# Optimization experiments

Hardware: AMD Instinct MI355X
Metric: run time of the kernel (lower is better)

The kernel has to match this reference:

```python
import jax, jax.numpy as jnp
import numpy as np

B, T, N, C = 32, 16, 1000, 16   # batch, seq_len, num_nodes, in_channels
G, H, O = 32, 512, 8            # gcn_hidden, lstm_hidden, output_dim
E_RAND = 8000                   # random edges; + N self loops -> E = 9000


def setup_inputs() -> dict:
    key = jax.random.key(0)
    ks = jax.random.split(key, 13)
    rng = np.random.default_rng(0)
    src = rng.integers(0, N, E_RAND)
    dst = rng.integers(0, N, E_RAND)
    loop = np.arange(N)
    edge_index = jnp.asarray(
        np.stack([np.concatenate([src, loop]), np.concatenate([dst, loop])]),
        dtype=jnp.int32)
    ew = np.concatenate([rng.uniform(0.5, 1.5, E_RAND), np.ones(N)]).astype(np.float32)

    def p(k, s, sc):
        return jax.random.normal(k, s, jnp.float32) * sc

    return {
        'x': p(ks[0], (B, T, N, C), 1.0),
        'edge_index': edge_index,
        'edge_weight': jnp.asarray(ew),
        'gcn_w': p(ks[1], (T, C, G), 0.1),
        'gcn_b': p(ks[2], (T, G), 0.02),
        'w_ih0': p(ks[3], (4 * H, N * G), 0.02),
        'w_hh0': p(ks[4], (4 * H, H), 0.02),
        'b_ih0': p(ks[5], (4 * H,), 0.02),
        'b_hh0': p(ks[6], (4 * H,), 0.02),
        'w_ih1': p(ks[7], (4 * H, H), 0.02),
        'w_hh1': p(ks[8], (4 * H, H), 0.02),
        'b_ih1': p(ks[9], (4 * H,), 0.02),
        'b_hh1': p(ks[10], (4 * H,), 0.02),
        'proj_w': p(ks[11], (O, H), 0.04),
        'proj_b': p(ks[12], (O,), 0.02),
    }


def _lstm_layer(inp, w_ih, w_hh, b_ih, b_hh):
    # inp: [B, T, D]; torch gate order i, f, g, o
    pre = jnp.einsum('btd,gd->btg', inp, w_ih) + b_ih + b_hh  # [B, T, 4H]
    h0 = jnp.zeros((inp.shape[0], w_hh.shape[1]), inp.dtype)

    def step(carry, x_t):
        h, c = carry
        gates = x_t + h @ w_hh.T
        i, f, g, o = jnp.split(gates, 4, axis=-1)
        c = jax.nn.sigmoid(f) * c + jax.nn.sigmoid(i) * jnp.tanh(g)
        h = jax.nn.sigmoid(o) * jnp.tanh(c)
        return (h, c), h

    _, hs = jax.lax.scan(step, (h0, h0), pre.transpose(1, 0, 2))  # [T, B, H]
    return hs.transpose(1, 0, 2)


def reference(x, edge_index, edge_weight, gcn_w, gcn_b,
              w_ih0, w_hh0, b_ih0, b_hh0,
              w_ih1, w_hh1, b_ih1, b_hh1, proj_w, proj_b):
    src, dst = edge_index[0], edge_index[1]
    # GCN symmetric normalization (self-loops already present in edge list)
    deg = jax.ops.segment_sum(edge_weight, dst, num_segments=N)
    dinv = jnp.where(deg > 0, jax.lax.rsqrt(jnp.maximum(deg, 1e-12)), 0.0)
    norm = dinv[src] * edge_weight * dinv[dst]  # [E]
    # per-timestep linear transform: distinct GCN weight per t
    xw = jnp.einsum('btni,tio->btno', x, gcn_w)  # [B, T, N, G]
    # gather from source nodes, scale, scatter-add into targets
    msg = xw[:, :, src, :] * norm[None, None, :, None]      # [B, T, E, G]
    agg = jnp.zeros_like(xw).at[:, :, dst, :].add(msg)      # [B, T, N, G]
    h = jax.nn.relu(agg + gcn_b[None, :, None, :])
    seq = h.reshape(B, T, N * G)                            # [B, T, N*G]
    out1 = _lstm_layer(seq, w_ih0, w_hh0, b_ih0, b_hh0)
    out2 = _lstm_layer(out1, w_ih1, w_hh1, b_ih1, b_hh1)
    last = out2[:, -1, :]                                   # [B, H]
    return last @ proj_w.T + proj_b                         # [B, O]
```

## Files before the change

### kernel.cpp

```cpp
#include <hip/hip_runtime.h>
#include <hip/hip_bf16.h>

typedef unsigned short u16;
typedef __bf16 bf16x8 __attribute__((ext_vector_type(8)));
typedef float f32x4 __attribute__((ext_vector_type(4)));
typedef unsigned short u16x8 __attribute__((ext_vector_type(8)));
typedef unsigned long long u64;

#define NB 32
#define NT 16
#define NN 1000
#define NC 16
#define NG 32
#define NH 512
#define NK 32000
#define BH (NB*NH)
#define LWG 64
#define LTH 384

__device__ __forceinline__ u16 f2bf(float f) {
    unsigned int u = __float_as_uint(f);
    unsigned int r = u + 0x7FFFu + ((u >> 16) & 1u);
    return (u16)(r >> 16);
}

__device__ __forceinline__ float sigmoidf(float x) { return 1.f / (1.f + __expf(-x)); }

__device__ __forceinline__ float dot4(float4 a, float4 b) {
    return a.x * b.x + a.y * b.y + a.z * b.z + a.w * b.w;
}

#define AT_LOAD(p)    __hip_atomic_load((p), __ATOMIC_RELAXED, __HIP_MEMORY_SCOPE_AGENT)
#define AT_STORE(p,v) __hip_atomic_store((p), (v), __ATOMIC_RELAXED, __HIP_MEMORY_SCOPE_AGENT)

#define GLOAD16(g, l) __builtin_amdgcn_global_load_lds( \
    (const __attribute__((address_space(1))) void*)(g),  \
    (__attribute__((address_space(3))) void*)(l), 16, 0, 0)

__global__ void graph_prep(const int* __restrict__ ei, const float* __restrict__ ew, int E,
                           int* __restrict__ rowptr, int* __restrict__ csr_src,
                           float* __restrict__ csr_nrm) {
    __shared__ float degs[NN];
    __shared__ float dinv[NN];
    __shared__ int cnt[NN];
    __shared__ int rp[NN + 1];
    int tid = threadIdx.x;
    for (int n = tid; n < NN; n += 1024) { degs[n] = 0.f; cnt[n] = 0; }
    __syncthreads();
    for (int e = tid; e < E; e += 1024) {
        int d = ei[E + e];
        atomicAdd(&degs[d], ew[e]);
        atomicAdd(&cnt[d], 1);
    }
    __syncthreads();
    for (int n = tid; n < NN; n += 1024) {
        float d = degs[n];
        dinv[n] = d > 0.f ? rsqrtf(fmaxf(d, 1e-12f)) : 0.f;
    }
    __syncthreads();
    if (tid == 0) {
        int acc = 0;
        for (int n = 0; n < NN; ++n) { rp[n] = acc; acc += cnt[n]; }
        rp[NN] = acc;
    }
    __syncthreads();
    for (int n = tid; n <= NN; n += 1024) rowptr[n] = rp[n];
    for (int n = tid; n < NN; n += 1024) cnt[n] = 0;
    __syncthreads();
    for (int e = tid; e < E; e += 1024) {
        int d = ei[E + e], s = ei[e];
        int pos = rp[d] + atomicAdd(&cnt[d], 1);
        csr_src[pos] = s;
        csr_nrm[pos] = dinv[s] * ew[e] * dinv[d];
    }
}

__global__ __launch_bounds__(1024) void gcn_fused(const float* __restrict__ x,
                                                  const float* __restrict__ gw,
                                                  const float* __restrict__ gb,
                                                  const int* __restrict__ rowptr,
                                                  const int* __restrict__ csr_src,
                                                  const float* __restrict__ csr_nrm,
                                                  u16* __restrict__ seq) {
    __shared__ float xwlds[NN * NG];
    __shared__ float wlds[NC * NG];
    __shared__ int rplds[NN + 1];
    int bt = blockIdx.x;
    int t = bt & 15;
    int tid = threadIdx.x;
    int g = tid & 31, grp = tid >> 5;

    for (int i = tid; i < NC * NG; i += 1024) wlds[i] = gw[t * NC * NG + i];
    for (int i = tid; i <= NN; i += 1024) rplds[i] = rowptr[i];
    __syncthreads();

    const float* xbt = x + (size_t)bt * NN * NC;
    for (int r = grp; r < NN; r += 32) {
        const float* xr = xbt + r * NC;
        float acc = 0.f;
#pragma unroll
        for (int i = 0; i < NC; ++i) acc += xr[i] * wlds[i * NG + g];
        xwlds[r * NG + g] = acc;
    }
    __syncthreads();

    float bias = gb[t * NG + g];
    u16* seqbt = seq + (size_t)bt * NK;
    for (int n = grp; n < NN; n += 32) {
        int p0 = rplds[n], p1 = rplds[n + 1];
        float acc = 0.f;
        for (int p = p0; p < p1; ++p)
            acc += csr_nrm[p] * xwlds[csr_src[p] * NG + g];
        seqbt[n * NG + g] = f2bf(fmaxf(acc + bias, 0.f));
    }
}

__global__ void wconv(const float4* __restrict__ in, ushort4* __restrict__ out, int n4) {
    for (int i = blockIdx.x * blockDim.x + threadIdx.x; i < n4; i += gridDim.x * blockDim.x) {
        float4 v = in[i];
        ushort4 o;
        o.x = f2bf(v.x); o.y = f2bf(v.y); o.z = f2bf(v.z); o.w = f2bf(v.w);
        out[i] = o;
    }
}

__global__ __launch_bounds__(256) void gemm_bt(const u16* __restrict__ A,
                                               const u16* __restrict__ Bw,
                                               float* __restrict__ part) {
    __shared__ __align__(16) u16 As[128 * 64];
    __shared__ __align__(16) u16 Bs[128 * 64];
    int tid = threadIdx.x;
    int lane = tid & 63, wid = tid >> 6;
    int wr = wid >> 1, wc = wid & 1;
    int tm = blockIdx.x * 128, tn = blockIdx.y * 128;
    int s = blockIdx.z;
    int ks0 = s * 62 + (s < 4 ? s : 4);
    int ksn = (s < 4) ? 63 : 62;

    int srow = tid >> 3;
    int schunk = tid & 7;

    const u16* ga = A + (size_t)(tm + srow) * NK + (size_t)ks0 * 64 + schunk * 8;
    const u16* gb = Bw + (size_t)(tn + srow) * NK + (size_t)ks0 * 64 + schunk * 8;
    u16* la = As + srow * 64 + schunk * 8;
    u16* lb = Bs + srow * 64 + schunk * 8;

    f32x4 acc[4][4];
#pragma unroll
    for (int i = 0; i < 4; ++i)
#pragma unroll
        for (int j = 0; j < 4; ++j) acc[i][j] = (f32x4){0.f, 0.f, 0.f, 0.f};

    int fr = lane & 15, kq = lane >> 4;
    const u16* arow = As + (wr * 64 + fr) * 64 + kq * 8;
    const u16* brow = Bs + (wc * 64 + fr) * 64 + kq * 8;

    for (int ks = 0; ks < ksn; ++ks) {
        __syncthreads();
#pragma unroll
        for (int q = 0; q < 4; ++q) {
            GLOAD16(ga + (size_t)q * 32 * NK, la + q * 32 * 64);
            GLOAD16(gb + (size_t)q * 32 * NK, lb + q * 32 * 64);
        }
        __syncthreads();
#pragma unroll
        for (int kk = 0; kk < 2; ++kk) {
            bf16x8 af[4], bv[4];
#pragma unroll
            for (int fm = 0; fm < 4; ++fm) af[fm] = *(const bf16x8*)(arow + fm * 1024 + kk * 32);
#pragma unroll
            for (int fn = 0; fn < 4; ++fn) bv[fn] = *(const bf16x8*)(brow + fn * 1024 + kk * 32);
#pragma unroll
            for (int fm = 0; fm < 4; ++fm)
#pragma unroll
                for (int fn = 0; fn < 4; ++fn)
                    acc[fm][fn] = __builtin_amdgcn_mfma_f32_16x16x32_bf16(af[fm], bv[fn], acc[fm][fn], 0, 0, 0);
        }
        ga += 64; gb += 64;
    }

    int rq = lane >> 4;
    size_t base = (size_t)s * 512 * 2048;
#pragma unroll
    for (int fm = 0; fm < 4; ++fm)
#pragma unroll
        for (int fn = 0; fn < 4; ++fn)
#pragma unroll
            for (int rr = 0; rr < 4; ++rr) {
                int m = tm + wr * 64 + fm * 16 + rq * 4 + rr;
                int n = tn + wc * 64 + fn * 16 + (lane & 15);
                part[base + (size_t)m * 2048 + n] = acc[fm][fn][rr];
            }
}

__global__ __launch_bounds__(256) void reduce_bias_p(const float* __restrict__ part,
                                                     const float* __restrict__ b_ih0,
                                                     const float* __restrict__ b_hh0,
                                                     float* __restrict__ pre0p) {
    int s = blockIdx.y;
    int r = blockIdx.x * 64 + (threadIdx.x & 63);
    int bq = threadIdx.x >> 6;
    float bias = b_ih0[r] + b_hh0[r];
#pragma unroll
    for (int b8 = 0; b8 < 8; ++b8) {
        int b = bq * 8 + b8;
        float acc = bias;
#pragma unroll
        for (int sk = 0; sk < 8; ++sk)
            acc += part[(size_t)sk * 1048576 + (size_t)(b * 16 + s) * 2048 + r];
        pre0p[((size_t)s * 2048 + r) * 32 + b] = acc;
    }
}

__global__ __launch_bounds__(256) void wperm(const float* __restrict__ w_hh0,
                                             const float* __restrict__ w_ih1,
                                             const float* __restrict__ w_hh1,
                                             u16* __restrict__ Wbig) {
    int rt = blockIdx.x;
    int wg = blockIdx.y;
    int tid = threadIdx.x;
#pragma unroll
    for (int it = 0; it < 4; ++it) {
        int idx = it * 256 + tid;
        int kt = idx >> 6, lane = idx & 63;
        int p = rt * 16 + (lane & 15);
        int gate = (p & 31) >> 3;
        int col = wg * 8 + (p & 7);
        const float* src;
        if (p < 32)      src = w_hh0 + (size_t)(gate * NH + col) * NH;
        else if (p < 64) src = w_ih1 + (size_t)(gate * NH + col) * NH;
        else             src = w_hh1 + (size_t)(gate * NH + col) * NH;
        int k0 = kt * 32 + (lane >> 4) * 8;
        float4 v0 = *(const float4*)(src + k0);
        float4 v1 = *(const float4*)(src + k0 + 4);
        u16x8 o;
        o[0] = f2bf(v0.x); o[1] = f2bf(v0.y); o[2] = f2bf(v0.z); o[3] = f2bf(v0.w);
        o[4] = f2bf(v1.x); o[5] = f2bf(v1.y); o[6] = f2bf(v1.z); o[7] = f2bf(v1.w);
        *(u16x8*)(Wbig + (((size_t)wg * 6 + rt) * 16 + kt) * 512 + lane * 8) = o;
    }
}

__global__ void init2(u16* h0, u16* h1, int* flags) {
    int i = blockIdx.x * 256 + threadIdx.x;
    if (i < 2 * BH) { h0[i] = 0; h1[i] = 0; }
    if (i < 1024) flags[i] = 0;
}

__global__ __launch_bounds__(LTH) void lstm2(const u16* __restrict__ Wbig,
                                             const float* __restrict__ pre0p,
                                             const float* __restrict__ b_ih1,
                                             const float* __restrict__ b_hh1,
                                             u16* __restrict__ h0buf,
                                             u16* __restrict__ h1buf,
                                             float* __restrict__ h1f,
                                             int* __restrict__ flags) {
    __shared__ __align__(16) u16 hA0[32 * 520];
    __shared__ __align__(16) u16 hA1[32 * 520];
    __shared__ float G[96][33];
    __shared__ float cst[2][8][32];
    __shared__ u16 hst[2][8][32];
    int wg = blockIdx.x, tid = threadIdx.x;
    int wid = tid >> 6, lane = tid & 63;
    int grp = wid >> 1;

    bf16x8 af[16];
    const u16* wsrc = Wbig + (size_t)wg * 49152 + wid * 8192 + lane * 8;
#pragma unroll
    for (int kt = 0; kt < 16; ++kt) af[kt] = *(const bf16x8*)(wsrc + kt * 512);

    if (tid < 512) ((float*)cst)[tid] = 0.f;

    int uj = (tid >> 5) & 7, ub = tid & 31;
    int ucol = wg * 8 + uj;
    float bs0 = 0.f, bs1 = 0.f, bs2 = 0.f, bs3 = 0.f;
    if (tid < 256) {
        bs0 = b_ih1[ucol] + b_hh1[ucol];
        bs1 = b_ih1[NH + ucol] + b_hh1[NH + ucol];
        bs2 = b_ih1[2 * NH + ucol] + b_hh1[2 * NH + ucol];
        bs3 = b_ih1[3 * NH + ucol] + b_hh1[3 * NH + ucol];
    }
    __syncthreads();

    for (int s = 0; s <= 16; ++s) {
        for (int r = wid; r < 64; r += 6) {
            const u64* src = (r < 32)
                ? (const u64*)(h0buf + ((s & 1) ^ 1) * BH + r * 512)
                : (const u64*)(h1buf + (s & 1) * BH + (r - 32) * 512);
            u16* dst = (r < 32) ? (hA0 + r * 520) : (hA1 + (r - 32) * 520);
            u64 v0 = AT_LOAD(src + lane);
            u64 v1 = AT_LOAD(src + 64 + lane);
            *(u64*)(dst + lane * 4) = v0;
            *(u64*)(dst + 256 + lane * 4) = v1;
        }
        float up0 = 0.f, up1 = 0.f, up2 = 0.f, up3 = 0.f;
        if (tid < 256 && s < 16) {
            const float* pp = pre0p + (size_t)s * 2048 * 32 + ub;
            up0 = pp[(size_t)ucol * 32];
            up1 = pp[((size_t)NH + ucol) * 32];
            up2 = pp[((size_t)2 * NH + ucol) * 32];
            up3 = pp[((size_t)3 * NH + ucol) * 32];
        }
        __syncthreads();

        bool active = (grp == 0) ? (s < 16) : (s >= 1);
        if (active) {
            const u16* hA = (grp < 2) ? hA0 : hA1;
            const u16* hp = hA + (lane & 15) * 520 + (lane >> 4) * 8;
            f32x4 a0 = (f32x4){0.f, 0.f, 0.f, 0.f};
            f32x4 a1 = (f32x4){0.f, 0.f, 0.f, 0.f};
#pragma unroll
            for (int kt = 0; kt < 16; ++kt) {
                bf16x8 b0 = *(const bf16x8*)(hp + kt * 32);
                bf16x8 b1 = *(const bf16x8*)(hp + 16 * 520 + kt * 32);
                a0 = __builtin_amdgcn_mfma_f32_16x16x32_bf16(af[kt], b0, a0, 0, 0, 0);
                a1 = __builtin_amdgcn_mfma_f32_16x16x32_bf16(af[kt], b1, a1, 0, 0, 0);
            }
            int r0 = wid * 16 + (lane >> 4) * 4;
#pragma unroll
            for (int rr = 0; rr < 4; ++rr) {
                G[r0 + rr][lane & 15] = a0[rr];
                G[r0 + rr][16 + (lane & 15)] = a1[rr];
            }
        }
        __syncthreads();

        if (tid < 256) {
            if (s < 16) {
                float gi = G[uj][ub] + up0;
                float gf = G[8 + uj][ub] + up1;
                float gg = G[16 + uj][ub] + up2;
                float go = G[24 + uj][ub] + up3;
                float c = sigmoidf(gf) * cst[0][uj][ub] + sigmoidf(gi) * tanhf(gg);
                cst[0][uj][ub] = c;
                hst[0][uj][ub] = f2bf(sigmoidf(go) * tanhf(c));
            }
            if (s >= 1) {
                float gi = G[32 + uj][ub] + G[64 + uj][ub] + bs0;
                float gf = G[40 + uj][ub] + G[72 + uj][ub] + bs1;
                float gg = G[48 + uj][ub] + G[80 + uj][ub] + bs2;
                float go = G[56 + uj][ub] + G[88 + uj][ub] + bs3;
                float c = sigmoidf(gf) * cst[1][uj][ub] + sigmoidf(gi) * tanhf(gg);
                cst[1][uj][ub] = c;
                float hv = sigmoidf(go) * tanhf(c);
                hst[1][uj][ub] = f2bf(hv);
                if (s == 16) h1f[ub * NH + ucol] = hv;
            }
        }
        __syncthreads();

        if (s < 16) {
            if (wid == 0) {
                if (lane < 32) {
                    union { u16 a[8]; u64 q[2]; } v;
#pragma unroll
                    for (int j = 0; j < 8; ++j) v.a[j] = hst[0][j][lane];
                    u64* d = (u64*)(h0buf + (s & 1) * BH + lane * 512 + wg * 8);
                    AT_STORE(d, v.q[0]); AT_STORE(d + 1, v.q[1]);
                } else if (s >= 1) {
                    int b = lane - 32;
                    union { u16 a[8]; u64 q[2]; } v;
#pragma unroll
                    for (int j = 0; j < 8; ++j) v.a[j] = hst[1][j][b];
                    u64* d = (u64*)(h1buf + ((s - 1) & 1) * BH + b * 512 + wg * 8);
                    AT_STORE(d, v.q[0]); AT_STORE(d + 1, v.q[1]);
                }
                asm volatile("s_waitcnt vmcnt(0)" ::: "memory");
                if (lane == 0) AT_STORE(&flags[wg * 16], s + 1);
                int target = s + 1;
                for (;;) {
                    int v = AT_LOAD(&flags[lane * 16]);
                    if (__all(v >= target)) break;
                    __builtin_amdgcn_s_sleep(2);
                }
            }
            __syncthreads();
        }
    }
}

__global__ __launch_bounds__(1024) void proj_k(const float* __restrict__ h1f,
                                               const float* __restrict__ proj_w,
                                               const float* __restrict__ proj_b,
                                               float* __restrict__ out) {
    __shared__ float pj[32][8][4];
    int tid = threadIdx.x;
    int b = tid >> 5, o = (tid >> 2) & 7, kq = tid & 3;
    const float4* hp = (const float4*)(h1f + (size_t)b * NH + kq * 128);
    const float4* wp = (const float4*)(proj_w + (size_t)o * NH + kq * 128);
    float acc = 0.f;
#pragma unroll 8
    for (int k = 0; k < 32; ++k) acc += dot4(hp[k], wp[k]);
    pj[b][o][kq] = acc;
    __syncthreads();
    if (tid < 256) {
        int bb = tid >> 3, oo = tid & 7;
        out[bb * 8 + oo] = pj[bb][oo][0] + pj[bb][oo][1] + pj[bb][oo][2] + pj[bb][oo][3] + proj_b[oo];
    }
}

extern "C" void kernel_launch(void* const* d_in, const int* in_sizes, int n_in,
                              void* d_out, int out_size, void* d_ws, size_t ws_size,
                              hipStream_t stream) {
    const float* x      = (const float*)d_in[0];
    const int*   ei     = (const int*)d_in[1];
    const float* ew     = (const float*)d_in[2];
    const float* gcn_w  = (const float*)d_in[3];
    const float* gcn_b  = (const float*)d_in[4];
    const float* w_ih0  = (const float*)d_in[5];
    const float* w_hh0  = (const float*)d_in[6];
    const float* b_ih0  = (const float*)d_in[7];
    const float* b_hh0  = (const float*)d_in[8];
    const float* w_ih1  = (const float*)d_in[9];
    const float* w_hh1  = (const float*)d_in[10];
    const float* b_ih1  = (const float*)d_in[11];
    const float* b_hh1  = (const float*)d_in[12];
    const float* proj_w = (const float*)d_in[13];
    const float* proj_b = (const float*)d_in[14];
    int E = in_sizes[2];

    char* ws = (char*)d_ws;
    size_t off = 0;
    u16* w16      = (u16*)(ws + off);  off += 131072000;
    float* part   = (float*)(ws + off);
    u16* Wbig     = (u16*)part;        off += 65536000;
    u16* seq      = (u16*)(ws + off);  off += 32768000;
    float* pre0p  = (float*)(ws + off); off += 4194304;
    u16* h0buf    = (u16*)(ws + off);  off += 2 * BH * 2;
    u16* h1buf    = (u16*)(ws + off);  off += 2 * BH * 2;
    float* h1f    = (float*)(ws + off); off += BH * 4;
    int* flags    = (int*)(ws + off);  off += 4096;
    int* rowptr   = (int*)(ws + off);  off += 4096;
    int* csr_src  = (int*)(ws + off);  off += 36864;
    float* csr_nrm = (float*)(ws + off); off += 36864;
    (void)ws_size; (void)n_in; (void)out_size;

    graph_prep<<<1, 1024, 0, stream>>>(ei, ew, E, rowptr, csr_src, csr_nrm);
    gcn_fused<<<512, 1024, 0, stream>>>(x, gcn_w, gcn_b, rowptr, csr_src, csr_nrm, seq);
    wconv<<<8192, 256, 0, stream>>>((const float4*)w_ih0, (ushort4*)w16, 16384000);
    gemm_bt<<<dim3(4, 16, 8), 256, 0, stream>>>(seq, w16, part);
    reduce_bias_p<<<dim3(32, 16), 256, 0, stream>>>(part, b_ih0, b_hh0, pre0p);
    wperm<<<dim3(6, 64), 256, 0, stream>>>(w_hh0, w_ih1, w_hh1, Wbig);
    init2<<<128, 256, 0, stream>>>(h0buf, h1buf, flags);

    lstm2<<<LWG, LTH, 0, stream>>>(Wbig, pre0p, b_ih1, b_hh1, h0buf, h1buf, h1f, flags);
    proj_k<<<1, 1024, 0, stream>>>(h1f, proj_w, proj_b, (float*)d_out);
}
```

Measured before the change: 507.0 us.

## Fuse fp32-to-bf16 weight conversion into GEMM B-tile load and raise split-K

Removes the separate wconv pass over the 65M-element fp32 w_ih0 and instead loads fp32 rows directly in the GEMM, converting them to bf16 with packed cvt instructions before storing to LDS. Split-K rises from 8 to 12 so more blocks are in flight. Graph prep replaces the serial prefix sum with a wave-shuffle scan, the GCN input transform uses float4 loads, and the LSTM spin-wait sleep is shortened. This avoids writing and rereading a 131MB bf16 copy, but B loads now pass through registers instead of async direct-to-LDS loads, and the partial sums buffer grows.

```diff
diff --git a/kernel.cpp b/kernel.cpp
--- a/kernel.cpp
+++ b/kernel.cpp
@@ -17,11 +17,18 @@
 #define BH (NB*NH)
 #define LWG 64
 #define LTH 384
+#define NSPLIT 12
 
 __device__ __forceinline__ u16 f2bf(float f) {
     unsigned int u = __float_as_uint(f);
     unsigned int r = u + 0x7FFFu + ((u >> 16) & 1u);
     return (u16)(r >> 16);
+}
+
+__device__ __forceinline__ unsigned cvt2(float a, float b) {
+    unsigned r;
+    asm("v_cvt_pk_bf16_f32 %0, %1, %2" : "=v"(r) : "v"(a), "v"(b));
+    return r;
 }
 
 __device__ __forceinline__ float sigmoidf(float x) { return 1.f / (1.f + __expf(-x)); }
@@ -44,7 +51,8 @@
     __shared__ float dinv[NN];
     __shared__ int cnt[NN];
     __shared__ int rp[NN + 1];
-    int tid = threadIdx.x;
+    __shared__ int wsum[16];
+    int tid = threadIdx.x, lane = tid & 63, wid = tid >> 6;
     for (int n = tid; n < NN; n += 1024) { degs[n] = 0.f; cnt[n] = 0; }
     __syncthreads();
     for (int e = tid; e < E; e += 1024) {
@@ -57,15 +65,24 @@
         float d = degs[n];
         dinv[n] = d > 0.f ? rsqrtf(fmaxf(d, 1e-12f)) : 0.f;
     }
+    int v = (tid < NN) ? cnt[tid] : 0;
+    int inc = v;
+#pragma unroll
+    for (int d = 1; d < 64; d <<= 1) {
+        int u = __shfl_up(inc, d, 64);
+        if (lane >= d) inc += u;
+    }
+    if (lane == 63) wsum[wid] = inc;
     __syncthreads();
     if (tid == 0) {
-        int acc = 0;
-        for (int n = 0; n < NN; ++n) { rp[n] = acc; acc += cnt[n]; }
-        rp[NN] = acc;
-    }
-    __syncthreads();
-    for (int n = tid; n <= NN; n += 1024) rowptr[n] = rp[n];
-    for (int n = tid; n < NN; n += 1024) cnt[n] = 0;
+        int a = 0;
+#pragma unroll
+        for (int i = 0; i < 16; ++i) { int t = wsum[i]; wsum[i] = a; a += t; }
+    }
+    __syncthreads();
+    int excl = inc - v + wsum[wid];
+    if (tid <= NN) { rp[tid] = excl; rowptr[tid] = excl; }
+    if (tid < NN) cnt[tid] = 0;
     __syncthreads();
     for (int e = tid; e < E; e += 1024) {
         int d = ei[E + e], s = ei[e];
@@ -96,10 +113,16 @@
 
     const float* xbt = x + (size_t)bt * NN * NC;
     for (int r = grp; r < NN; r += 32) {
-        const float* xr = xbt + r * NC;
-        float acc = 0.f;
-#pragma unroll
-        for (int i = 0; i < NC; ++i) acc += xr[i] * wlds[i * NG + g];
+        const float4* xr = (const float4*)(xbt + r * NC);
+        float4 a0 = xr[0], a1 = xr[1], a2 = xr[2], a3 = xr[3];
+        float acc = a0.x * wlds[g]        + a0.y * wlds[32 + g]
+                  + a0.z * wlds[64 + g]   + a0.w * wlds[96 + g]
+                  + a1.x * wlds[128 + g]  + a1.y * wlds[160 + g]
+                  + a1.z * wlds[192 + g]  + a1.w * wlds[224 + g]
+                  + a2.x * wlds[256 + g]  + a2.y * wlds[288 + g]
+                  + a2.z * wlds[320 + g]  + a2.w * wlds[352 + g]
+                  + a3.x * wlds[384 + g]  + a3.y * wlds[416 + g]
+                  + a3.z * wlds[448 + g]  + a3.w * wlds[480 + g];
         xwlds[r * NG + g] = acc;
     }
     __syncthreads();
@@ -115,18 +138,9 @@
     }
 }
 
-__global__ void wconv(const float4* __restrict__ in, ushort4* __restrict__ out, int n4) {
-    for (int i = blockIdx.x * blockDim.x + threadIdx.x; i < n4; i += gridDim.x * blockDim.x) {
-        float4 v = in[i];
-        ushort4 o;
-        o.x = f2bf(v.x); o.y = f2bf(v.y); o.z = f2bf(v.z); o.w = f2bf(v.w);
-        out[i] = o;
-    }
-}
-
-__global__ __launch_bounds__(256) void gemm_bt(const u16* __restrict__ A,
-                                               const u16* __restrict__ Bw,
-                                               float* __restrict__ part) {
+__global__ __launch_bounds__(256) void gemm_f32b(const u16* __restrict__ A,
+                                                 const float* __restrict__ Bw,
+                                                 float* __restrict__ part) {
     __shared__ __align__(16) u16 As[128 * 64];
     __shared__ __align__(16) u16 Bs[128 * 64];
     int tid = threadIdx.x;
@@ -134,16 +148,19 @@
     int wr = wid >> 1, wc = wid & 1;
     int tm = blockIdx.x * 128, tn = blockIdx.y * 128;
     int s = blockIdx.z;
-    int ks0 = s * 62 + (s < 4 ? s : 4);
-    int ksn = (s < 4) ? 63 : 62;
+    int ks0 = (s < 8) ? s * 42 : 336 + (s - 8) * 41;
+    int ksn = (s < 8) ? 42 : 41;
 
     int srow = tid >> 3;
     int schunk = tid & 7;
 
     const u16* ga = A + (size_t)(tm + srow) * NK + (size_t)ks0 * 64 + schunk * 8;
-    const u16* gb = Bw + (size_t)(tn + srow) * NK + (size_t)ks0 * 64 + schunk * 8;
     u16* la = As + srow * 64 + schunk * 8;
-    u16* lb = Bs + srow * 64 + schunk * 8;
+
+    int brow = tid >> 1;
+    int bhalf = tid & 1;
+    const float* gbf = Bw + (size_t)(tn + brow) * NK + (size_t)ks0 * 64 + bhalf * 32;
+    u16* lb = Bs + brow * 64 + bhalf * 32;
 
     f32x4 acc[4][4];
 #pragma unroll
@@ -153,14 +170,35 @@
 
     int fr = lane & 15, kq = lane >> 4;
     const u16* arow = As + (wr * 64 + fr) * 64 + kq * 8;
-    const u16* brow = Bs + (wc * 64 + fr) * 64 + kq * 8;
+    const u16* brw  = Bs + (wc * 64 + fr) * 64 + kq * 8;
 
     for (int ks = 0; ks < ksn; ++ks) {
         __syncthreads();
 #pragma unroll
-        for (int q = 0; q < 4; ++q) {
+        for (int q = 0; q < 4; ++q)
             GLOAD16(ga + (size_t)q * 32 * NK, la + q * 32 * 64);
-            GLOAD16(gb + (size_t)q * 32 * NK, lb + q * 32 * 64);
+        {
+            float4 q0 = *(const float4*)(gbf + 0);
+            float4 q1 = *(const float4*)(gbf + 4);
+            float4 q2 = *(const float4*)(gbf + 8);
+            float4 q3 = *(const float4*)(gbf + 12);
+            float4 q4 = *(const float4*)(gbf + 16);
+            float4 q5 = *(const float4*)(gbf + 20);
+            float4 q6 = *(const float4*)(gbf + 24);
+            float4 q7 = *(const float4*)(gbf + 28);
+            uint4 w0, w1;
+            w0.x = cvt2(q0.x, q0.y); w0.y = cvt2(q0.z, q0.w);
+            w0.z = cvt2(q1.x, q1.y); w0.w = cvt2(q1.z, q1.w);
+            w1.x = cvt2(q2.x, q2.y); w1.y = cvt2(q2.z, q2.w);
+            w1.z = cvt2(q3.x, q3.y); w1.w = cvt2(q3.z, q3.w);
+            *(uint4*)(lb) = w0;
+            *(uint4*)(lb + 8) = w1;
+            w0.x = cvt2(q4.x, q4.y); w0.y = cvt2(q4.z, q4.w);
+            w0.z = cvt2(q5.x, q5.y); w0.w = cvt2(q5.z, q5.w);
+            w1.x = cvt2(q6.x, q6.y); w1.y = cvt2(q6.z, q6.w);
+            w1.z = cvt2(q7.x, q7.y); w1.w = cvt2(q7.z, q7.w);
+            *(uint4*)(lb + 16) = w0;
+            *(uint4*)(lb + 24) = w1;
         }
         __syncthreads();
 #pragma unroll
@@ -169,14 +207,14 @@
 #pragma unroll
             for (int fm = 0; fm < 4; ++fm) af[fm] = *(const bf16x8*)(arow + fm * 1024 + kk * 32);
 #pragma unroll
-            for (int fn = 0; fn < 4; ++fn) bv[fn] = *(const bf16x8*)(brow + fn * 1024 + kk * 32);
+            for (int fn = 0; fn < 4; ++fn) bv[fn] = *(const bf16x8*)(brw + fn * 1024 + kk * 32);
 #pragma unroll
             for (int fm = 0; fm < 4; ++fm)
 #pragma unroll
                 for (int fn = 0; fn < 4; ++fn)
                     acc[fm][fn] = __builtin_amdgcn_mfma_f32_16x16x32_bf16(af[fm], bv[fn], acc[fm][fn], 0, 0, 0);
         }
-        ga += 64; gb += 64;
+        ga += 64; gbf += 64;
     }
 
     int rq = lane >> 4;
@@ -206,7 +244,7 @@
         int b = bq * 8 + b8;
         float acc = bias;
 #pragma unroll
-        for (int sk = 0; sk < 8; ++sk)
+        for (int sk = 0; sk < NSPLIT; ++sk)
             acc += part[(size_t)sk * 1048576 + (size_t)(b * 16 + s) * 2048 + r];
         pre0p[((size_t)s * 2048 + r) * 32 + b] = acc;
     }
@@ -370,7 +408,7 @@
                 for (;;) {
                     int v = AT_LOAD(&flags[lane * 16]);
                     if (__all(v >= target)) break;
-                    __builtin_amdgcn_s_sleep(2);
+                    __builtin_amdgcn_s_sleep(1);
                 }
             }
             __syncthreads();
@@ -420,9 +458,8 @@
 
     char* ws = (char*)d_ws;
     size_t off = 0;
-    u16* w16      = (u16*)(ws + off);  off += 131072000;
     float* part   = (float*)(ws + off);
-    u16* Wbig     = (u16*)part;        off += 65536000;
+    u16* Wbig     = (u16*)part;        off += 50331648;
     u16* seq      = (u16*)(ws + off);  off += 32768000;
     float* pre0p  = (float*)(ws + off); off += 4194304;
     u16* h0buf    = (u16*)(ws + off);  off += 2 * BH * 2;
@@ -436,8 +473,7 @@
 
     graph_prep<<<1, 1024, 0, stream>>>(ei, ew, E, rowptr, csr_src, csr_nrm);
     gcn_fused<<<512, 1024, 0, stream>>>(x, gcn_w, gcn_b, rowptr, csr_src, csr_nrm, seq);
-    wconv<<<8192, 256, 0, stream>>>((const float4*)w_ih0, (ushort4*)w16, 16384000);
-    gemm_bt<<<dim3(4, 16, 8), 256, 0, stream>>>(seq, w16, part);
+    gemm_f32b<<<dim3(4, 16, NSPLIT), 256, 0, stream>>>(seq, w_ih0, part);
     reduce_bias_p<<<dim3(32, 16), 256, 0, stream>>>(part, b_ih0, b_hh0, pre0p);
     wperm<<<dim3(6, 64), 256, 0, stream>>>(w_hh0, w_ih1, w_hh1, Wbig);
     init2<<<128, 256, 0, stream>>>(h0buf, h1buf, flags);
```

After: 559.4 us. +10.3%, slower.
